# Kernel tuning notes

Hardware: AMD Instinct MI355X
Metric: run time of the kernel (lower is better)

## Reference

```python
import jax, jax.numpy as jnp
import numpy as np

EPS = 1e-5

def layer_norm(x, w, b):
    m = jnp.mean(x, axis=-1, keepdims=True)
    v = jnp.mean(jnp.square(x - m), axis=-1, keepdims=True)
    return (x - m) * jax.lax.rsqrt(v + EPS) * w + b

def setup_inputs() -> dict:
    key = jax.random.key(0)
    B, S, D, H = 4, 2048, 768, 12
    Dh, F = D // H, 4 * D
    ks = jax.random.split(key, 16)
    s = 0.02
    return {
        "x":    jax.random.normal(ks[0], (B, S, D), dtype=jnp.float32),
        # per-head q/k/v projections stacked over heads: [H, D, Dh]
        "Wq":   jax.random.normal(ks[1], (H, D, Dh), dtype=jnp.float32) * s,
        "bq":   jnp.zeros((H, Dh), dtype=jnp.float32),
        "Wk":   jax.random.normal(ks[2], (H, D, Dh), dtype=jnp.float32) * s,
        "bk":   jnp.zeros((H, Dh), dtype=jnp.float32),
        "Wv":   jax.random.normal(ks[3], (H, D, Dh), dtype=jnp.float32) * s,
        "bv":   jnp.zeros((H, Dh), dtype=jnp.float32),
        "Wo":   jax.random.normal(ks[4], (D, D), dtype=jnp.float32) * s,
        "bo":   jnp.zeros((D,), dtype=jnp.float32),
        "W1":   jax.random.normal(ks[5], (D, F), dtype=jnp.float32) * s,
        "b1":   jnp.zeros((F,), dtype=jnp.float32),
        "W2":   jax.random.normal(ks[6], (F, D), dtype=jnp.float32) * s,
        "b2":   jnp.zeros((D,), dtype=jnp.float32),
        "ln1_w": jnp.ones((D,), dtype=jnp.float32),
        "ln1_b": jnp.zeros((D,), dtype=jnp.float32),
        "ln2_w": jnp.ones((D,), dtype=jnp.float32),
        "ln2_b": jnp.zeros((D,), dtype=jnp.float32),
    }

def reference(x, Wq, bq, Wk, bk, Wv, bv, Wo, bo, W1, b1, W2, b2,
              ln1_w, ln1_b, ln2_w, ln2_b):
    B, S, D = x.shape
    H, _, Dh = Wq.shape
    scale = jnp.sqrt(jnp.float32(Dh))  # torch scales by sqrt(dout)
    # q,k,v: [B, H, S, Dh]
    q = jnp.einsum('bsd,hde->bhse', x, Wq) + bq[None, :, None, :]
    k = jnp.einsum('bsd,hde->bhse', x, Wk) + bk[None, :, None, :]
    v = jnp.einsum('bsd,hde->bhse', x, Wv) + bv[None, :, None, :]
    scores = jnp.einsum('bhqe,bhke->bhqk', q, k) / scale  # [B,H,S,S]
    causal = jnp.tril(jnp.ones((S, S), dtype=bool))
    scores = jnp.where(causal[None, None], scores, -jnp.inf)
    attn = jax.nn.softmax(scores, axis=-1)
    ctx = jnp.einsum('bhqk,bhke->bhqe', attn, v)           # [B,H,S,Dh]
    ctx = jnp.transpose(ctx, (0, 2, 1, 3)).reshape(B, S, D)  # concat heads
    att_out = ctx @ Wo + bo
    h = layer_norm(x + att_out, ln1_w, ln1_b)  # post-norm, dropout=0
    ff = jax.nn.gelu(h @ W1 + b1, approximate=False) @ W2 + b2
    return layer_norm(h + ff, ln2_w, ln2_b)
```

## Files before the change

kernel.cpp:

```cpp
#include <hip/hip_runtime.h>
#include <hip/hip_bf16.h>
#include <math.h>

#define B_ 4
#define S_ 2048
#define D_ 768
#define H_ 12
#define DH_ 64
#define F_ 3072
#define NTOK (B_*S_)
#define BH_ (B_*H_)

typedef __hip_bfloat16 bf16;
typedef __attribute__((ext_vector_type(8))) short bf16x8;
typedef __attribute__((ext_vector_type(4))) float f32x4;
typedef __attribute__((ext_vector_type(4))) _Float16 half4;
typedef __attribute__((ext_vector_type(8))) _Float16 half8;
typedef __attribute__((ext_vector_type(2))) __fp16 fp16x2;

#define GLD16(g, l) __builtin_amdgcn_global_load_lds( \
    (__attribute__((address_space(1))) void*)(uintptr_t)(g), \
    (__attribute__((address_space(3))) void*)(uintptr_t)(l), 16, 0, 0)

__device__ __forceinline__ float bs2f(short s){
  union { unsigned int u; float f; } cv; cv.u = ((unsigned int)(unsigned short)s) << 16; return cv.f;
}
__device__ __forceinline__ float b2f(bf16 v){ return __bfloat162float(v); }
__device__ __forceinline__ bf16 f2b(float v){ return __float2bfloat16(v); }
__device__ __forceinline__ short f2bb(float v){ bf16 b = f2b(v); short s; __builtin_memcpy(&s, &b, 2); return s; }

__device__ __forceinline__ half4 pk4(float p0, float p1, float p2, float p3){
  union { fp16x2 v2[2]; half4 v4; } u;
  u.v2[0] = __builtin_amdgcn_cvt_pkrtz(p0, p1);
  u.v2[1] = __builtin_amdgcn_cvt_pkrtz(p2, p3);
  return u.v4;
}

__device__ __forceinline__ void wgbar(){
  __builtin_amdgcn_s_barrier();
  asm volatile("" ::: "memory");
}
__device__ __forceinline__ void wgbar_lds(){
  asm volatile("s_waitcnt lgkmcnt(0)" ::: "memory");
  __builtin_amdgcn_s_barrier();
  asm volatile("" ::: "memory");
}

__device__ __forceinline__ float gelu_fast(float v){
  const float c0 = -2.302208157f;
  const float c1 = -0.102943238f;
  float w = v*v;
  float z = v * __builtin_fmaf(c1, w, c0);
  float t = __builtin_amdgcn_exp2f(z);
  return v * __builtin_amdgcn_rcpf(1.0f + t);
}

__global__ __launch_bounds__(256) void prep_k(
    const float4* __restrict__ x4, short4* __restrict__ xb4,
    const float* __restrict__ Wo, bf16* __restrict__ WoT,
    const float* __restrict__ W1, bf16* __restrict__ W1T,
    const float* __restrict__ W2, bf16* __restrict__ W2T,
    const float* __restrict__ Wq, const float* __restrict__ bq,
    const float* __restrict__ Wk, const float* __restrict__ bk,
    const float* __restrict__ Wv, const float* __restrict__ bv,
    bf16* __restrict__ Wt, float* __restrict__ bcat)
{
  __shared__ float t[32][33];
  int bid = blockIdx.x;
  const int tidx = threadIdx.x;

  if (bid < 6144){
    const int i = bid*256 + tidx;
    float4 v = x4[i];
    short4 o;
    o.x = f2bb(v.x); o.y = f2bb(v.y); o.z = f2bb(v.z); o.w = f2bb(v.w);
    xb4[i] = o;
    return;
  }
  bid -= 6144;
  if (bid >= 576 + 2304 + 2304){
    bid -= 576 + 2304 + 2304;
    const int idx = bid*256 + tidx;
    {
      int n = idx / D_;
      int k = idx - n*D_;
      int which = n / D_;
      int cc = n - which*D_;
      int h = cc >> 6, e = cc & 63;
      const float* W = (which==0) ? Wq : ((which==1) ? Wk : Wv);
      Wt[idx] = f2b(W[((size_t)h*D_ + k)*DH_ + e]);
    }
    if (idx < 3*D_){
      int which = idx / D_;
      int cc = idx - which*D_;
      int h = cc >> 6, e = cc & 63;
      const float* bb = (which==0) ? bq : ((which==1) ? bk : bv);
      bcat[idx] = bb[h*DH_ + e];
    }
    return;
  }
  const float* tin; bf16* tout; int K, N, tiles_x;
  if (bid < 576){ tin = Wo; tout = WoT; K = D_; N = D_; tiles_x = 24; }
  else if (bid < 576 + 2304){ bid -= 576; tin = W1; tout = W1T; K = D_; N = F_; tiles_x = 96; }
  else { bid -= 576 + 2304; tin = W2; tout = W2T; K = F_; N = D_; tiles_x = 24; }
  const int kb = (bid / tiles_x)*32, nb = (bid % tiles_x)*32;
  const int xx = tidx & 31, y = tidx >> 5;
#pragma unroll
  for (int yy = y; yy < 32; yy += 8)
    t[yy][xx] = tin[(size_t)(kb+yy)*N + nb + xx];
  __syncthreads();
#pragma unroll
  for (int yy = y; yy < 32; yy += 8)
    tout[(size_t)(nb+yy)*K + kb + xx] = f2b(t[xx][yy]);
}

template<int EPI>
__global__ __launch_bounds__(256) void mgemm128_k(
    const bf16* __restrict__ A, const bf16* __restrict__ Bt,
    const float* __restrict__ bias, const bf16* __restrict__ aux,
    bf16* __restrict__ C, int M, int N, int K,
    bf16* __restrict__ qb, bf16* __restrict__ kbuf, _Float16* __restrict__ vt)
{
  __shared__ __align__(16) bf16 As[16384];
  __shared__ __align__(16) bf16 Bs[16384];
  const int tid  = threadIdx.x;
  const int wave = tid >> 6, lane = tid & 63;
  const int quad = lane >> 4, l16 = lane & 15;
  const int wm = (wave >> 1) * 64, wn = (wave & 1) * 64;

  const int NX = gridDim.x;
  const int f  = blockIdx.y * NX + blockIdx.x;
  const int xcd = f & 7;
  const int j   = f >> 3;
  const int bx  = j % NX;
  const int by  = (j / NX) * 8 + xcd;
  const int m0 = by * 128, n0 = bx * 128;

  const int srow8 = lane >> 3;
  const int g     = (lane & 7) ^ srow8;
  const bf16* gA = A  + (size_t)(m0 + wave*32 + srow8)*K + g*8;
  const bf16* gB = Bt + (size_t)(n0 + wave*32 + srow8)*K + g*8;
  const uintptr_t asb = (uintptr_t)(void*)As + (size_t)wave*32*128;
  const uintptr_t bsb = (uintptr_t)(void*)Bs + (size_t)wave*32*128;

  f32x4 acc[4][4];
#pragma unroll
  for (int i=0;i<4;i++)
#pragma unroll
    for (int j2=0;j2<4;j2++) acc[i][j2] = (f32x4)0.f;

  const char* AsB = (const char*)As;
  const char* BsB = (const char*)Bs;
  const int KT = K >> 6;

#pragma unroll
  for (int t=0;t<4;t++){
    GLD16(gA + (size_t)t*8*K, asb + t*1024);
    GLD16(gB + (size_t)t*8*K, bsb + t*1024);
  }
  gA += 64; gB += 64;
  asm volatile("s_waitcnt vmcnt(0)" ::: "memory");
  wgbar();

  for (int kt = 0; kt < KT; ++kt){
    const int cur = kt & 1, nxt = cur ^ 1;
    const bool pf = (kt + 1) < KT;
    if (pf){
      const uintptr_t ao = asb + (size_t)nxt*16384;
      const uintptr_t bo = bsb + (size_t)nxt*16384;
#pragma unroll
      for (int t=0;t<4;t++){
        GLD16(gA + (size_t)t*8*K, ao + t*1024);
        GLD16(gB + (size_t)t*8*K, bo + t*1024);
      }
      gA += 64; gB += 64;
    }
    const char* Ac = AsB + (size_t)cur*16384;
    const char* Bc = BsB + (size_t)cur*16384;
#pragma unroll
    for (int kq = 0; kq < 2; kq++){
      const int cbase = kq*4 + quad;
      bf16x8 af[4], bfr[4];
#pragma unroll
      for (int i=0;i<4;i++){
        const int m = wm + i*16 + l16;
        af[i] = *(const bf16x8*)(Ac + (m << 7) + ((cbase ^ (m & 7)) << 4));
      }
#pragma unroll
      for (int j2=0;j2<4;j2++){
        const int n = wn + j2*16 + l16;
        bfr[j2] = *(const bf16x8*)(Bc + (n << 7) + ((cbase ^ (n & 7)) << 4));
      }
#pragma unroll
      for (int i=0;i<4;i++)
#pragma unroll
        for (int j2=0;j2<4;j2++)
          acc[i][j2] = __builtin_amdgcn_mfma_f32_16x16x32_bf16(af[i], bfr[j2], acc[i][j2], 0, 0, 0);
    }
    if (pf) asm volatile("s_waitcnt vmcnt(0)" ::: "memory");
    wgbar();
  }

#pragma unroll
  for (int i=0;i<4;i++){
#pragma unroll
    for (int j2=0;j2<4;j2++){
      const int n = n0 + wn + j2*16 + l16;
      const int m_base = m0 + wm + i*16 + quad*4;
      if (EPI == 0){
        const int which = n / D_;
        const int cc = n - which*D_;
        const int h = cc >> 6, e = cc & 63;
        if (which == 2){
          const int b = m_base >> 11, s = m_base & (S_-1);
          const int sl = s & 63;
          const int perm = ((sl>>2)&3)*16 + ((sl>>4)&3)*4;
          half4 hv;
#pragma unroll
          for (int r=0;r<4;r++) hv[r] = (_Float16)(acc[i][j2][r] + bias[n]);
          *(half4*)(vt + ((size_t)(b*H_+h)*DH_ + e)*S_ + (s & ~63) + perm) = hv;
        } else {
          bf16* dst = (which==0) ? qb : kbuf;
          const float sc2 = (which==0) ? 0.18033688f : 1.0f;
#pragma unroll
          for (int r=0;r<4;r++){
            const int m = m_base + r;
            const int b = m >> 11, s = m & (S_-1);
            dst[((size_t)(b*H_+h)*S_ + s)*DH_ + e] = f2b((acc[i][j2][r] + bias[n]) * sc2);
          }
        }
      } else if (EPI == 1){
#pragma unroll
        for (int r=0;r<4;r++){
          const int m = m_base + r;
          float v = acc[i][j2][r] + bias[n] + b2f(aux[(size_t)m*N + n]);
          C[(size_t)m*N + n] = f2b(v);
        }
      } else {
#pragma unroll
        for (int r=0;r<4;r++){
          const int m = m_base + r;
          float v = acc[i][j2][r] + bias[n];
          C[(size_t)m*N + n] = f2b(gelu_fast(v));
        }
      }
    }
  }
}

__global__ __launch_bounds__(256, 4) void fattn_k(const bf16* __restrict__ qb,
    const bf16* __restrict__ kb, const _Float16* __restrict__ vt, bf16* __restrict__ ctx)
{
  __shared__ __align__(16) char smem[36864];
  typedef bf16     KsRow[72];
  typedef _Float16 VsRow[72];
  KsRow* kp0 = (KsRow*)(smem);
  KsRow* kp1 = (KsRow*)(smem + 9216);
  VsRow* vp0 = (VsRow*)(smem + 18432);
  VsRow* vp1 = (VsRow*)(smem + 27648);

  const int bh = blockIdx.x;
  const int qt = 31 - blockIdx.y;
  const int q0 = qt * 64;
  const int tid = threadIdx.x;
  const int wave = tid >> 6, lane = tid & 63;
  const int quad = lane >> 4, l16 = lane & 15;
  const size_t kbase = (size_t)bh * S_ * DH_;
  const int nt = qt + 1;

  const int sr  = tid >> 2;
  const int seg = (tid & 3) * 16;

  const int qloc = wave*16 + l16;
  bf16x8 qf[2];
#pragma unroll
  for (int h=0; h<2; h++)
    qf[h] = *(const bf16x8*)(qb + kbase + (size_t)(q0 + qloc)*DH_ + h*32 + quad*8);

  f32x4 o[4];
#pragma unroll
  for (int df=0; df<4; df++) o[df] = (f32x4)0.f;
  float mi = -1e30f, li = 0.f;

  bf16x8 ka0, ka1; half8 va0, va1;
  {
    const bf16* ks = kb + kbase + (size_t)sr*DH_ + seg;
    ka0 = *(const bf16x8*)ks; ka1 = *(const bf16x8*)(ks + 8);
    const _Float16* vs = vt + ((size_t)bh*DH_ + sr)*S_ + seg;
    va0 = *(const half8*)vs; va1 = *(const half8*)(vs + 8);
  }
  *(bf16x8*)&kp0[sr][seg]   = ka0;
  *(bf16x8*)&kp0[sr][seg+8] = ka1;
  *(half8*)&vp0[sr][seg]    = va0;
  *(half8*)&vp0[sr][seg+8]  = va1;
  if (nt > 1){
    const bf16* ks = kb + kbase + (size_t)(64 + sr)*DH_ + seg;
    ka0 = *(const bf16x8*)ks; ka1 = *(const bf16x8*)(ks + 8);
    const _Float16* vs = vt + ((size_t)bh*DH_ + sr)*S_ + 64 + seg;
    va0 = *(const half8*)vs; va1 = *(const half8*)(vs + 8);
  }
  wgbar_lds();

  for (int kt = 0; kt < nt; ++kt){
    f32x4 sc[4];
#pragma unroll
    for (int mf=0; mf<4; mf++){
      bf16x8 a0 = *(const bf16x8*)&kp0[mf*16 + l16][quad*8];
      bf16x8 a1 = *(const bf16x8*)&kp0[mf*16 + l16][32 + quad*8];
      f32x4 t = __builtin_amdgcn_mfma_f32_16x16x32_bf16(a0, qf[0], (f32x4)0.f, 0, 0, 0);
      sc[mf]  = __builtin_amdgcn_mfma_f32_16x16x32_bf16(a1, qf[1], t, 0, 0, 0);
    }

    if (kt == qt){
#pragma unroll
      for (int mf=0; mf<4; mf++){
        const int keyl = mf*16 + quad*4;
#pragma unroll
        for (int r=0; r<4; r++)
          if (keyl + r > qloc) sc[mf][r] = -1e30f;
      }
    }

    float mx = -1e30f;
#pragma unroll
    for (int mf=0; mf<4; mf++)
#pragma unroll
      for (int r=0; r<4; r++) mx = fmaxf(mx, sc[mf][r]);
    mx = fmaxf(mx, __shfl_xor(mx, 16));
    mx = fmaxf(mx, __shfl_xor(mx, 32));

    half8 vva[4], vvb[4];
#pragma unroll
    for (int df=0; df<4; df++){
      vva[df] = *(const half8*)&vp0[df*16 + l16][quad*16];
      vvb[df] = *(const half8*)&vp0[df*16 + l16][quad*16 + 8];
    }

    if (kt + 1 < nt){
      *(bf16x8*)&kp1[sr][seg]   = ka0;
      *(bf16x8*)&kp1[sr][seg+8] = ka1;
      *(half8*)&vp1[sr][seg]    = va0;
      *(half8*)&vp1[sr][seg+8]  = va1;
      if (kt + 2 < nt){
        const int k0n = (kt + 2) * 64;
        const bf16* ks = kb + kbase + (size_t)(k0n + sr)*DH_ + seg;
        ka0 = *(const bf16x8*)ks; ka1 = *(const bf16x8*)(ks + 8);
        const _Float16* vs = vt + ((size_t)bh*DH_ + sr)*S_ + k0n + seg;
        va0 = *(const half8*)vs; va1 = *(const half8*)(vs + 8);
      }
    }
    wgbar_lds();

    const bool need = !__all(mx - mi <= 8.f);
    if (need){
      const float mn = fmaxf(mi, mx);
      const float a = __builtin_amdgcn_exp2f(mi - mn);
      mi = mn; li *= a;
#pragma unroll
      for (int df=0; df<4; df++)
#pragma unroll
        for (int r=0; r<4; r++) o[df][r] *= a;
    }

    half4 pfr[4];
    float rs = 0.f;
#pragma unroll
    for (int mf=0; mf<4; mf++){
      const float p0 = __builtin_amdgcn_exp2f(sc[mf][0] - mi);
      const float p1 = __builtin_amdgcn_exp2f(sc[mf][1] - mi);
      const float p2 = __builtin_amdgcn_exp2f(sc[mf][2] - mi);
      const float p3 = __builtin_amdgcn_exp2f(sc[mf][3] - mi);
      rs += (p0 + p1) + (p2 + p3);
      pfr[mf] = pk4(p0, p1, p2, p3);
    }
    rs += __shfl_xor(rs, 16);
    rs += __shfl_xor(rs, 32);
    li += rs;

#pragma unroll
    for (int df=0; df<4; df++){
      half4 k0f = __builtin_shufflevector(vva[df], vva[df], 0,1,2,3);
      half4 k1f = __builtin_shufflevector(vva[df], vva[df], 4,5,6,7);
      half4 k2f = __builtin_shufflevector(vvb[df], vvb[df], 0,1,2,3);
      half4 k3f = __builtin_shufflevector(vvb[df], vvb[df], 4,5,6,7);
      o[df] = __builtin_amdgcn_mfma_f32_16x16x16f16(k0f, pfr[0], o[df], 0, 0, 0);
      o[df] = __builtin_amdgcn_mfma_f32_16x16x16f16(k1f, pfr[1], o[df], 0, 0, 0);
      o[df] = __builtin_amdgcn_mfma_f32_16x16x16f16(k2f, pfr[2], o[df], 0, 0, 0);
      o[df] = __builtin_amdgcn_mfma_f32_16x16x16f16(k3f, pfr[3], o[df], 0, 0, 0);
    }

    { KsRow* t_ = kp0; kp0 = kp1; kp1 = t_; }
    { VsRow* t_ = vp0; vp0 = vp1; vp1 = t_; }
  }

  const int b = bh / H_, h = bh - (bh / H_)*H_;
  const float inv = 1.0f / li;
  const int token = q0 + qloc;
  short* cdst = (short*)ctx + ((size_t)(b*S_ + token))*D_ + h*DH_;
#pragma unroll
  for (int df=0; df<4; df++){
    short4 pk;
    pk.x = f2bb(o[df][0] * inv);
    pk.y = f2bb(o[df][1] * inv);
    pk.z = f2bb(o[df][2] * inv);
    pk.w = f2bb(o[df][3] * inv);
    *(short4*)(cdst + df*16 + quad*4) = pk;
  }
}

template<typename T> __device__ __forceinline__ void st4(T* p, size_t idx, float a, float b, float c, float d);
template<> __device__ __forceinline__ void st4<float>(float* p, size_t idx, float a, float b, float c, float d){
  float4 v; v.x=a; v.y=b; v.z=c; v.w=d; *(float4*)(p+idx) = v;
}
template<> __device__ __forceinline__ void st4<bf16>(bf16* p, size_t idx, float a, float b, float c, float d){
  short4 v; v.x=f2bb(a); v.y=f2bb(b); v.z=f2bb(c); v.w=f2bb(d); *(short4*)((short*)p+idx) = v;
}

template<typename OutT>
__global__ __launch_bounds__(192) void layernorm_k(const bf16* __restrict__ X,
    const float* __restrict__ g, const float* __restrict__ bta, OutT* __restrict__ Y)
{
  const int row = blockIdx.x;
  const int tid = threadIdx.x;
  const short4 raw = *(const short4*)((const short*)X + (size_t)row*D_ + tid*4);
  const float v0 = bs2f(raw.x), v1 = bs2f(raw.y), v2 = bs2f(raw.z), v3 = bs2f(raw.w);
  float s  = v0+v1+v2+v3;
  float s2 = v0*v0+v1*v1+v2*v2+v3*v3;
#pragma unroll
  for (int o = 32; o > 0; o >>= 1){ s += __shfl_down(s, o); s2 += __shfl_down(s2, o); }
  __shared__ float rs[3], rq[3];
  const int lane = tid & 63, w = tid >> 6;
  if (lane == 0){ rs[w] = s; rq[w] = s2; }
  __syncthreads();
  s  = rs[0]+rs[1]+rs[2];
  s2 = rq[0]+rq[1]+rq[2];
  const float mean = s * (1.0f/D_);
  const float var  = s2 * (1.0f/D_) - mean*mean;
  const float inv  = rsqrtf(var + 1e-5f);
  const float4 g4 = *(const float4*)(g + tid*4);
  const float4 b4 = *(const float4*)(bta + tid*4);
  st4(Y, (size_t)row*D_ + tid*4,
      (v0-mean)*inv*g4.x + b4.x,
      (v1-mean)*inv*g4.y + b4.y,
      (v2-mean)*inv*g4.z + b4.z,
      (v3-mean)*inv*g4.w + b4.w);
}

extern "C" void kernel_launch(void* const* d_in, const int* in_sizes, int n_in,
                              void* d_out, int out_size, void* d_ws, size_t ws_size,
                              hipStream_t stream)
{
  const float* x   = (const float*)d_in[0];
  const float* Wq  = (const float*)d_in[1];
  const float* bq  = (const float*)d_in[2];
  const float* Wk  = (const float*)d_in[3];
  const float* bk  = (const float*)d_in[4];
  const float* Wv  = (const float*)d_in[5];
  const float* bv  = (const float*)d_in[6];
  const float* Wo  = (const float*)d_in[7];
  const float* bo  = (const float*)d_in[8];
  const float* W1  = (const float*)d_in[9];
  const float* b1  = (const float*)d_in[10];
  const float* W2  = (const float*)d_in[11];
  const float* b2  = (const float*)d_in[12];
  const float* g1  = (const float*)d_in[13];
  const float* be1 = (const float*)d_in[14];
  const float* g2  = (const float*)d_in[15];
  const float* be2 = (const float*)d_in[16];
  float* out = (float*)d_out;

  char* ws = (char*)d_ws;
  size_t off = 0;
  auto alloc = [&](size_t bytes)->char*{
    char* p = ws + off; off = (off + bytes + 255) & ~(size_t)255; return p;
  };
  bf16*  xb    = (bf16*) alloc((size_t)NTOK*D_*2);
  bf16*  WcatT = (bf16*) alloc((size_t)3*D_*D_*2);
  float* bcat  = (float*)alloc((size_t)3*D_*4);
  bf16*  WoT   = (bf16*) alloc((size_t)D_*D_*2);
  bf16*  W1T   = (bf16*) alloc((size_t)F_*D_*2);
  bf16*  W2T   = (bf16*) alloc((size_t)D_*F_*2);
  bf16*  r1    = (bf16*) alloc((size_t)NTOK*F_*2);
  bf16*  qb    = r1;
  bf16*  kb    = r1 + (size_t)NTOK*D_;
  _Float16* vt = (_Float16*)(r1 + (size_t)2*NTOK*D_);
  bf16*  ff1   = r1;
  bf16*  ctxb  = (bf16*) alloc((size_t)NTOK*D_*2);
  bf16*  y1    = (bf16*) alloc((size_t)NTOK*D_*2);
  bf16*  hb    = (bf16*) alloc((size_t)NTOK*D_*2);
  bf16*  y2    = ctxb;

  prep_k<<<18240, 256, 0, stream>>>(
      (const float4*)x, (short4*)xb, Wo, WoT, W1, W1T, W2, W2T,
      Wq, bq, Wk, bk, Wv, bv, WcatT, bcat);

  mgemm128_k<0><<<dim3(3*D_/128, NTOK/128), 256, 0, stream>>>(
      xb, WcatT, bcat, nullptr, nullptr, NTOK, 3*D_, D_, qb, kb, vt);

  fattn_k<<<dim3(BH_, S_/64), 256, 0, stream>>>(qb, kb, vt, ctxb);

  mgemm128_k<1><<<dim3(D_/128, NTOK/128), 256, 0, stream>>>(
      ctxb, WoT, bo, xb, y1, NTOK, D_, D_, nullptr, nullptr, nullptr);

  layernorm_k<bf16><<<NTOK, 192, 0, stream>>>(y1, g1, be1, hb);

  mgemm128_k<2><<<dim3(F_/128, NTOK/128), 256, 0, stream>>>(
      hb, W1T, b1, nullptr, ff1, NTOK, F_, D_, nullptr, nullptr, nullptr);

  mgemm128_k<1><<<dim3(D_/128, NTOK/128), 256, 0, stream>>>(
      ff1, W2T, b2, hb, y2, NTOK, D_, F_, nullptr, nullptr, nullptr);

  layernorm_k<float><<<NTOK, 192, 0, stream>>>(y2, g2, be2, out);
}
```

Baseline: 341.7 us.

## Use 128-query attention tiles with 8 waves and 16x16x32 f16 PV MFMA

```diff
diff --git a/kernel.cpp b/kernel.cpp
--- a/kernel.cpp
+++ b/kernel.cpp
@@ -214,7 +214,7 @@
         if (which == 2){
           const int b = m_base >> 11, s = m_base & (S_-1);
           const int sl = s & 63;
-          const int perm = ((sl>>2)&3)*16 + ((sl>>4)&3)*4;
+          const int perm = (sl & 32) | (((sl >> 2) & 3) << 3) | ((sl & 16) >> 2);
           half4 hv;
 #pragma unroll
           for (int r=0;r<4;r++) hv[r] = (_Float16)(acc[i][j2][r] + bias[n]);
@@ -248,7 +248,7 @@
   }
 }
 
-__global__ __launch_bounds__(256, 4) void fattn_k(const bf16* __restrict__ qb,
+__global__ __launch_bounds__(512, 4) void fattn_k(const bf16* __restrict__ qb,
     const bf16* __restrict__ kb, const _Float16* __restrict__ vt, bf16* __restrict__ ctx)
 {
   __shared__ __align__(16) char smem[36864];
@@ -260,133 +260,127 @@
   VsRow* vp1 = (VsRow*)(smem + 27648);
 
   const int bh = blockIdx.x;
-  const int qt = 31 - blockIdx.y;
-  const int q0 = qt * 64;
+  const int qt = 15 - blockIdx.y;
+  const int q0 = qt * 128;
   const int tid = threadIdx.x;
   const int wave = tid >> 6, lane = tid & 63;
   const int quad = lane >> 4, l16 = lane & 15;
   const size_t kbase = (size_t)bh * S_ * DH_;
-  const int nt = qt + 1;
-
-  const int sr  = tid >> 2;
-  const int seg = (tid & 3) * 16;
+  const int nt = 2*(qt + 1);
+
+  const int sr  = tid >> 3;
+  const int seg = (tid & 7) * 8;
 
   const int qloc = wave*16 + l16;
+  const int qglob = q0 + qloc;
   bf16x8 qf[2];
 #pragma unroll
   for (int h=0; h<2; h++)
-    qf[h] = *(const bf16x8*)(qb + kbase + (size_t)(q0 + qloc)*DH_ + h*32 + quad*8);
+    qf[h] = *(const bf16x8*)(qb + kbase + (size_t)qglob*DH_ + h*32 + quad*8);
 
   f32x4 o[4];
 #pragma unroll
   for (int df=0; df<4; df++) o[df] = (f32x4)0.f;
   float mi = -1e30f, li = 0.f;
 
-  bf16x8 ka0, ka1; half8 va0, va1;
+  bf16x8 ka; half8 va;
   {
     const bf16* ks = kb + kbase + (size_t)sr*DH_ + seg;
-    ka0 = *(const bf16x8*)ks; ka1 = *(const bf16x8*)(ks + 8);
+    ka = *(const bf16x8*)ks;
     const _Float16* vs = vt + ((size_t)bh*DH_ + sr)*S_ + seg;
-    va0 = *(const half8*)vs; va1 = *(const half8*)(vs + 8);
-  }
-  *(bf16x8*)&kp0[sr][seg]   = ka0;
-  *(bf16x8*)&kp0[sr][seg+8] = ka1;
-  *(half8*)&vp0[sr][seg]    = va0;
-  *(half8*)&vp0[sr][seg+8]  = va1;
+    va = *(const half8*)vs;
+  }
+  *(bf16x8*)&kp0[sr][seg] = ka;
+  *(half8*)&vp0[sr][seg]  = va;
   if (nt > 1){
-    const bf16* ks = kb + kbase + (size_t)(64 + sr)*DH_ + seg;
-    ka0 = *(const bf16x8*)ks; ka1 = *(const bf16x8*)(ks + 8);
-    const _Float16* vs = vt + ((size_t)bh*DH_ + sr)*S_ + 64 + seg;
-    va0 = *(const half8*)vs; va1 = *(const half8*)(vs + 8);
+    ka = *(const bf16x8*)(kb + kbase + (size_t)sr*DH_ + 64*DH_ + seg);
+    va = *(const half8*)(vt + ((size_t)bh*DH_ + sr)*S_ + 64 + seg);
   }
   wgbar_lds();
 
   for (int kt = 0; kt < nt; ++kt){
+    const int k0 = kt << 6;
+    const bool active = k0 <= q0 + wave*16 + 15;
+
     f32x4 sc[4];
-#pragma unroll
-    for (int mf=0; mf<4; mf++){
-      bf16x8 a0 = *(const bf16x8*)&kp0[mf*16 + l16][quad*8];
-      bf16x8 a1 = *(const bf16x8*)&kp0[mf*16 + l16][32 + quad*8];
-      f32x4 t = __builtin_amdgcn_mfma_f32_16x16x32_bf16(a0, qf[0], (f32x4)0.f, 0, 0, 0);
-      sc[mf]  = __builtin_amdgcn_mfma_f32_16x16x32_bf16(a1, qf[1], t, 0, 0, 0);
-    }
-
-    if (kt == qt){
+    half8 vva[4], vvb[4];
+    float mx = -1e30f;
+    if (active){
 #pragma unroll
       for (int mf=0; mf<4; mf++){
-        const int keyl = mf*16 + quad*4;
-#pragma unroll
-        for (int r=0; r<4; r++)
-          if (keyl + r > qloc) sc[mf][r] = -1e30f;
-      }
-    }
-
-    float mx = -1e30f;
-#pragma unroll
-    for (int mf=0; mf<4; mf++)
-#pragma unroll
-      for (int r=0; r<4; r++) mx = fmaxf(mx, sc[mf][r]);
-    mx = fmaxf(mx, __shfl_xor(mx, 16));
-    mx = fmaxf(mx, __shfl_xor(mx, 32));
-
-    half8 vva[4], vvb[4];
-#pragma unroll
-    for (int df=0; df<4; df++){
-      vva[df] = *(const half8*)&vp0[df*16 + l16][quad*16];
-      vvb[df] = *(const half8*)&vp0[df*16 + l16][quad*16 + 8];
+        bf16x8 a0 = *(const bf16x8*)&kp0[mf*16 + l16][quad*8];
+        bf16x8 a1 = *(const bf16x8*)&kp0[mf*16 + l16][32 + quad*8];
+        f32x4 t = __builtin_amdgcn_mfma_f32_16x16x32_bf16(a0, qf[0], (f32x4)0.f, 0, 0, 0);
+        sc[mf]  = __builtin_amdgcn_mfma_f32_16x16x32_bf16(a1, qf[1], t, 0, 0, 0);
+      }
+      if (k0 + 63 > q0 + wave*16){
+#pragma unroll
+        for (int mf=0; mf<4; mf++){
+          const int keyg = k0 + mf*16 + quad*4;
+#pragma unroll
+          for (int r=0; r<4; r++)
+            if (keyg + r > qglob) sc[mf][r] = -1e30f;
+        }
+      }
+#pragma unroll
+      for (int mf=0; mf<4; mf++)
+#pragma unroll
+        for (int r=0; r<4; r++) mx = fmaxf(mx, sc[mf][r]);
+      mx = fmaxf(mx, __shfl_xor(mx, 16));
+      mx = fmaxf(mx, __shfl_xor(mx, 32));
+
+#pragma unroll
+      for (int df=0; df<4; df++){
+        vva[df] = *(const half8*)&vp0[df*16 + l16][quad*8];
+        vvb[df] = *(const half8*)&vp0[df*16 + l16][32 + quad*8];
+      }
     }
 
     if (kt + 1 < nt){
-      *(bf16x8*)&kp1[sr][seg]   = ka0;
-      *(bf16x8*)&kp1[sr][seg+8] = ka1;
-      *(half8*)&vp1[sr][seg]    = va0;
-      *(half8*)&vp1[sr][seg+8]  = va1;
+      *(bf16x8*)&kp1[sr][seg] = ka;
+      *(half8*)&vp1[sr][seg]  = va;
       if (kt + 2 < nt){
-        const int k0n = (kt + 2) * 64;
-        const bf16* ks = kb + kbase + (size_t)(k0n + sr)*DH_ + seg;
-        ka0 = *(const bf16x8*)ks; ka1 = *(const bf16x8*)(ks + 8);
-        const _Float16* vs = vt + ((size_t)bh*DH_ + sr)*S_ + k0n + seg;
-        va0 = *(const half8*)vs; va1 = *(const half8*)(vs + 8);
+        const int k0n = (kt + 2) << 6;
+        ka = *(const bf16x8*)(kb + kbase + (size_t)(k0n + sr)*DH_ + seg);
+        va = *(const half8*)(vt + ((size_t)bh*DH_ + sr)*S_ + k0n + seg);
       }
     }
     wgbar_lds();
 
-    const bool need = !__all(mx - mi <= 8.f);
-    if (need){
-      const float mn = fmaxf(mi, mx);
-      const float a = __builtin_amdgcn_exp2f(mi - mn);
-      mi = mn; li *= a;
-#pragma unroll
-      for (int df=0; df<4; df++)
-#pragma unroll
-        for (int r=0; r<4; r++) o[df][r] *= a;
-    }
-
-    half4 pfr[4];
-    float rs = 0.f;
-#pragma unroll
-    for (int mf=0; mf<4; mf++){
-      const float p0 = __builtin_amdgcn_exp2f(sc[mf][0] - mi);
-      const float p1 = __builtin_amdgcn_exp2f(sc[mf][1] - mi);
-      const float p2 = __builtin_amdgcn_exp2f(sc[mf][2] - mi);
-      const float p3 = __builtin_amdgcn_exp2f(sc[mf][3] - mi);
-      rs += (p0 + p1) + (p2 + p3);
-      pfr[mf] = pk4(p0, p1, p2, p3);
-    }
-    rs += __shfl_xor(rs, 16);
-    rs += __shfl_xor(rs, 32);
-    li += rs;
-
-#pragma unroll
-    for (int df=0; df<4; df++){
-      half4 k0f = __builtin_shufflevector(vva[df], vva[df], 0,1,2,3);
-      half4 k1f = __builtin_shufflevector(vva[df], vva[df], 4,5,6,7);
-      half4 k2f = __builtin_shufflevector(vvb[df], vvb[df], 0,1,2,3);
-      half4 k3f = __builtin_shufflevector(vvb[df], vvb[df], 4,5,6,7);
-      o[df] = __builtin_amdgcn_mfma_f32_16x16x16f16(k0f, pfr[0], o[df], 0, 0, 0);
-      o[df] = __builtin_amdgcn_mfma_f32_16x16x16f16(k1f, pfr[1], o[df], 0, 0, 0);
-      o[df] = __builtin_amdgcn_mfma_f32_16x16x16f16(k2f, pfr[2], o[df], 0, 0, 0);
-      o[df] = __builtin_amdgcn_mfma_f32_16x16x16f16(k3f, pfr[3], o[df], 0, 0, 0);
+    if (active){
+      const bool need = !__all(mx - mi <= 8.f);
+      if (need){
+        const float mn = fmaxf(mi, mx);
+        const float a = __builtin_amdgcn_exp2f(mi - mn);
+        mi = mn; li *= a;
+#pragma unroll
+        for (int df=0; df<4; df++)
+#pragma unroll
+          for (int r=0; r<4; r++) o[df][r] *= a;
+      }
+
+      half4 pfr[4];
+      float rs = 0.f;
+#pragma unroll
+      for (int mf=0; mf<4; mf++){
+        const float p0 = __builtin_amdgcn_exp2f(sc[mf][0] - mi);
+        const float p1 = __builtin_amdgcn_exp2f(sc[mf][1] - mi);
+        const float p2 = __builtin_amdgcn_exp2f(sc[mf][2] - mi);
+        const float p3 = __builtin_amdgcn_exp2f(sc[mf][3] - mi);
+        rs += (p0 + p1) + (p2 + p3);
+        pfr[mf] = pk4(p0, p1, p2, p3);
+      }
+      rs += __shfl_xor(rs, 16);
+      rs += __shfl_xor(rs, 32);
+      li += rs;
+
+      half8 p01 = __builtin_shufflevector(pfr[0], pfr[1], 0,1,2,3,4,5,6,7);
+      half8 p23 = __builtin_shufflevector(pfr[2], pfr[3], 0,1,2,3,4,5,6,7);
+#pragma unroll
+      for (int df=0; df<4; df++){
+        o[df] = __builtin_amdgcn_mfma_f32_16x16x32_f16(vva[df], p01, o[df], 0, 0, 0);
+        o[df] = __builtin_amdgcn_mfma_f32_16x16x32_f16(vvb[df], p23, o[df], 0, 0, 0);
+      }
     }
 
     { KsRow* t_ = kp0; kp0 = kp1; kp1 = t_; }
@@ -395,8 +389,7 @@
 
   const int b = bh / H_, h = bh - (bh / H_)*H_;
   const float inv = 1.0f / li;
-  const int token = q0 + qloc;
-  short* cdst = (short*)ctx + ((size_t)(b*S_ + token))*D_ + h*DH_;
+  short* cdst = (short*)ctx + ((size_t)(b*S_ + qglob))*D_ + h*DH_;
 #pragma unroll
   for (int df=0; df<4; df++){
     short4 pk;
@@ -497,7 +490,7 @@
   mgemm128_k<0><<<dim3(3*D_/128, NTOK/128), 256, 0, stream>>>(
       xb, WcatT, bcat, nullptr, nullptr, NTOK, 3*D_, D_, qb, kb, vt);
 
-  fattn_k<<<dim3(BH_, S_/64), 256, 0, stream>>>(qb, kb, vt, ctxb);
+  fattn_k<<<dim3(BH_, S_/128), 512, 0, stream>>>(qb, kb, vt, ctxb);
 
   mgemm128_k<1><<<dim3(D_/128, NTOK/128), 256, 0, stream>>>(
       ctxb, WoT, bo, xb, y1, NTOK, D_, D_, nullptr, nullptr, nullptr);
```

New measurement: 359.0 us. 5.1% more time.
